# Performance work log

Hardware: AMD Instinct MI355X
Metric: run time of the kernel (lower is better)

Reference implementation:

```python
import jax, jax.numpy as jnp
import numpy as np

NL = 6        # num_layers
V = 512       # pad_vocab_size (d_model)
H = 8         # nhead
HD = V // H   # head dim
DFF = 2048    # dim_feedforward
MAXLEN = 1024 # max distance for relative-position embedding
B = 8
L = 1024
EPS = 1e-5


def _ln(x, g, b):
    m = jnp.mean(x, axis=-1, keepdims=True)
    v = jnp.mean(jnp.square(x - m), axis=-1, keepdims=True)
    return (x - m) * jax.lax.rsqrt(v + EPS) * g + b


def setup_inputs() -> dict:
    key = jax.random.key(0)
    ks = jax.random.split(key, 16)
    s = 0.02
    rn = lambda k, shp: (jax.random.normal(k, shp) * s).astype(jnp.float32)
    return {
        "x": jax.random.uniform(ks[0], (B, L, V), jnp.float32),
        "dist_emb": rn(ks[1], (MAXLEN + 1, H)),
        "in_proj_w": rn(ks[2], (NL, 3 * V, V)),
        "in_proj_b": rn(ks[3], (NL, 3 * V)),
        "out_w": rn(ks[4], (NL, V, V)),
        "out_b": rn(ks[5], (NL, V)),
        "lin1_w": rn(ks[6], (NL, DFF, V)),
        "lin1_b": rn(ks[7], (NL, DFF)),
        "lin2_w": rn(ks[8], (NL, V, DFF)),
        "lin2_b": rn(ks[9], (NL, V)),
        "ln1_g": jnp.ones((NL, V), jnp.float32),
        "ln1_b": jnp.zeros((NL, V), jnp.float32),
        "ln2_g": jnp.ones((NL, V), jnp.float32),
        "ln2_b": jnp.zeros((NL, V), jnp.float32),
        "lnf_g": jnp.ones((V,), jnp.float32),
        "lnf_b": jnp.zeros((V,), jnp.float32),
    }


def _forward(x, dist_emb, in_proj_w, in_proj_b, out_w, out_b,
             lin1_w, lin1_b, lin2_w, lin2_b,
             ln1_g, ln1_b, ln2_g, ln2_b, lnf_g, lnf_b):
    bsz, seqlen, _ = x.shape
    idx = jnp.arange(seqlen)
    dist = jnp.clip(jnp.abs(idx[None, :] - idx[:, None]), 0, MAXLEN)  # (L, L)
    bias = jnp.transpose(dist_emb[dist], (2, 0, 1))[None]  # (1, H, L, L)
    causal = idx[None, :] <= idx[:, None]                   # allow j <= i
    bias = jnp.where(causal[None, None], bias, -jnp.inf)
    kpm = ~jnp.any(x != 0, axis=2)                          # (B, L) key padding
    bias = jnp.where(kpm[:, None, None, :], -jnp.inf, bias)  # (B, H, L, L)

    out = x  # eval mode: dropouts are identity
    scale = 1.0 / np.sqrt(HD)
    for l in range(NL):
        # --- self attention (post-norm TransformerEncoderLayer) ---
        qkv = out @ in_proj_w[l].T + in_proj_b[l]            # (B, L, 3V)
        q, k, v = jnp.split(qkv, 3, axis=-1)
        q = q.reshape(bsz, seqlen, H, HD)
        k = k.reshape(bsz, seqlen, H, HD)
        v = v.reshape(bsz, seqlen, H, HD)
        scores = jnp.einsum('bqhd,bkhd->bhqk', q, k) * scale + bias
        probs = jax.nn.softmax(scores, axis=-1)
        attn = jnp.einsum('bhqk,bkhd->bqhd', probs, v).reshape(bsz, seqlen, V)
        attn = attn @ out_w[l].T + out_b[l]
        out = _ln(out + attn, ln1_g[l], ln1_b[l])
        # --- feed forward (gelu) ---
        h = jax.nn.gelu(out @ lin1_w[l].T + lin1_b[l], approximate=False)
        ff = h @ lin2_w[l].T + lin2_b[l]
        out = _ln(out + ff, ln2_g[l], ln2_b[l])
    return _ln(out, lnf_g, lnf_b)


def reference(x, dist_emb, in_proj_w, in_proj_b, out_w, out_b,
              lin1_w, lin1_b, lin2_w, lin2_b,
              ln1_g, ln1_b, ln2_g, ln2_b, lnf_g, lnf_b):
    return _forward(x, dist_emb, in_proj_w, in_proj_b, out_w, out_b,
                    lin1_w, lin1_b, lin2_w, lin2_b,
                    ln1_g, ln1_b, ln2_g, ln2_b, lnf_g, lnf_b)
```

## Files before the change

kernel.cpp:

```cpp
#include <hip/hip_runtime.h>
#include <hip/hip_bf16.h>
#include <math.h>

#define NL 6
#define V 512
#define H 8
#define HD 64
#define DFF 2048
#define MAXLEN 1024
#define B 8
#define L 1024
#define M (B*L)
#define EPS 1e-5f
#define LOG2E 1.44269504088896f

typedef __hip_bfloat16 bf16;
typedef __attribute__((ext_vector_type(8))) short s8v;
typedef __attribute__((ext_vector_type(4))) float f4v;

__device__ __forceinline__ float b2f(bf16 v){ return __bfloat162float(v); }
__device__ __forceinline__ bf16 f2b(float v){ return __float2bfloat16(v); }
__device__ __forceinline__ unsigned short f2bu(float v){
  return __builtin_bit_cast(unsigned short, __float2bfloat16(v));
}
__device__ __forceinline__ float usf(unsigned short u){
  union{unsigned int i; float f;} c; c.i = ((unsigned int)u)<<16; return c.f;
}

__device__ __forceinline__ float ldin(const void* p, size_t i, int bf){
  if(bf) return b2f(((const bf16*)p)[i]);
  return ((const float*)p)[i];
}

__device__ __forceinline__ void ldin8f(const void* p, size_t e, int bf, float* o){
  if(bf){
    union{uint4 v; unsigned short u[8];} c;
    c.v = *(const uint4*)((const bf16*)p + e);
    #pragma unroll
    for(int i=0;i<8;i++) o[i]=usf(c.u[i]);
  }else{
    const float* f=(const float*)p+e;
    float4 a=*(const float4*)f, b=*(const float4*)(f+4);
    o[0]=a.x;o[1]=a.y;o[2]=a.z;o[3]=a.w;o[4]=b.x;o[5]=b.y;o[6]=b.z;o[7]=b.w;
  }
}

__device__ __forceinline__ uint4 ldw8(const void* W, size_t e, int bf){
  if(bf) return *(const uint4*)((const bf16*)W + e);
  const float* p = (const float*)W + e;
  float4 f0 = *(const float4*)p;
  float4 f1 = *(const float4*)(p+4);
  union { unsigned short u[8]; uint4 v; } r;
  r.u[0]=f2bu(f0.x); r.u[1]=f2bu(f0.y); r.u[2]=f2bu(f0.z); r.u[3]=f2bu(f0.w);
  r.u[4]=f2bu(f1.x); r.u[5]=f2bu(f1.y); r.u[6]=f2bu(f1.z); r.u[7]=f2bu(f1.w);
  return r.v;
}

__device__ __forceinline__ void async16(const bf16* g, unsigned short* l){
  __builtin_amdgcn_global_load_lds((const __attribute__((address_space(1))) void*)g,
                                   (__attribute__((address_space(3))) void*)l, 16, 0, 0);
}

__global__ void k_detect(const void* ones, int* flag){
  unsigned int u = *(const unsigned int*)ones;
  flag[0] = (u == 0x3F803F80u) ? 1 : 0;
  flag[1] = 1;
}

__global__ __launch_bounds__(256) void k_conv(const void* __restrict__ src,
                                              bf16* __restrict__ dst,
                                              const int* __restrict__ flag, int n){
  int bf = *flag;
  int e = (blockIdx.x*256 + threadIdx.x)*8;
  if(e >= n) return;
  if(bf){
    *(uint4*)(dst+e) = *(const uint4*)((const bf16*)src + e);
  }else{
    const float* s = (const float*)src + e;
    float4 a = *(const float4*)s, b2 = *(const float4*)(s+4);
    union{uint4 v; unsigned short u[8];} c;
    c.u[0]=f2bu(a.x); c.u[1]=f2bu(a.y); c.u[2]=f2bu(a.z); c.u[3]=f2bu(a.w);
    c.u[4]=f2bu(b2.x);c.u[5]=f2bu(b2.y);c.u[6]=f2bu(b2.z);c.u[7]=f2bu(b2.w);
    *(uint4*)(dst+e) = c.v;
  }
}

__global__ __launch_bounds__(256) void k_cast_kpm(const void* __restrict__ x,
                                                 const int* __restrict__ flag,
                                                 bf16* __restrict__ cur,
                                                 float* __restrict__ kpm){
  int bf = *flag;
  int row = blockIdx.x; int t = threadIdx.x;
  __shared__ int nz;
  if(t==0) nz = 0;
  __syncthreads();
  int fl = 0;
  for(int e=t; e<V; e+=256){
    float f = ldin(x, (size_t)row*V+e, bf);
    cur[(size_t)row*V+e] = f2b(f);
    if(f != 0.f) fl = 1;
  }
  if(fl) atomicOr(&nz, 1);
  __syncthreads();
  if(t==0) kpm[row] = nz ? 0.f : 1.f;
}

template<int BN, int WM, int WN, int TM, int TN>
__global__ __launch_bounds__(256) void k_gemm(const bf16* __restrict__ A,
                                              const void* __restrict__ W,
                                              const void* __restrict__ bias,
                                              const int* __restrict__ flag,
                                              bf16* __restrict__ C,
                                              int Ndim, int K, int gelu,
                                              size_t w_off, size_t b_off){
  constexpr int TILE = (128+BN)*64;
  constexpr int ES  = BN + 8;
  __shared__ unsigned short lds[2*TILE];
  int bf = *flag;
  int t = threadIdx.x;
  int rb = blockIdx.x*128, cb = blockIdx.y*BN;
  int lane = t & 63, w = t >> 6;
  int wm = w % WM, wn = w / WM;
  int quad = lane >> 4, fid = lane & 15;

  f4v acc[TM][TN];
  #pragma unroll
  for(int i=0;i<TM;i++)
    #pragma unroll
    for(int j=0;j<TN;j++){ f4v z = {0.f,0.f,0.f,0.f}; acc[i][j] = z; }

  auto stage = [&](int kt, int bsel){
    unsigned short* Ad = lds + bsel*TILE;
    unsigned short* Bd = Ad + 128*64;
    int k0 = kt*64;
    #pragma unroll
    for(int i=0;i<4;i++){
      int r = w*32 + i*8 + (lane>>3);
      const bf16* g = A + (size_t)(rb+r)*K + k0 + (((lane&7)^(r&7))<<3);
      async16(g, Ad + (w*32 + i*8)*64);
    }
    if(bf){
      #pragma unroll
      for(int i=0;i<BN/32;i++){
        int r = w*(BN/4) + i*8 + (lane>>3);
        const bf16* g = (const bf16*)W + w_off + (size_t)(cb+r)*K + k0 + (((lane&7)^(r&7))<<3);
        async16(g, Bd + (w*(BN/4) + i*8)*64);
      }
    }else{
      const int tpr = 256/BN;
      int sr = t/tpr;
      int sc0 = (t%tpr)*(64/tpr);
      #pragma unroll
      for(int c=0;c<64/tpr;c+=8){
        uint4 d = ldw8(W, w_off + (size_t)(cb+sr)*K + k0 + sc0 + c, 0);
        int chunk = (sc0+c)>>3;
        *(uint4*)&Bd[sr*64 + ((chunk^(sr&7))<<3)] = d;
      }
    }
  };

  int KT = K/64;
  stage(0, 0);
  __syncthreads();
  int cur = 0;
  for(int kt=0;kt<KT;kt++){
    if(kt+1<KT) stage(kt+1, cur^1);
    unsigned short* As = lds + cur*TILE;
    unsigned short* Bs = As + 128*64;
    #pragma unroll
    for(int h=0;h<2;h++){
      s8v av[TM], bv[TN];
      #pragma unroll
      for(int tm=0;tm<TM;tm++){
        int r = wm*(TM*16) + tm*16 + fid;
        av[tm] = *(const s8v*)&As[r*64 + (((h*4+quad)^(r&7))<<3)];
      }
      #pragma unroll
      for(int tn=0;tn<TN;tn++){
        int c = wn*(TN*16) + tn*16 + fid;
        bv[tn] = *(const s8v*)&Bs[c*64 + (((h*4+quad)^(c&7))<<3)];
      }
      #pragma unroll
      for(int tm=0;tm<TM;tm++)
        #pragma unroll
        for(int tn=0;tn<TN;tn++)
          acc[tm][tn] = __builtin_amdgcn_mfma_f32_16x16x32_bf16(av[tm], bv[tn], acc[tm][tn], 0,0,0);
    }
    __syncthreads();
    cur ^= 1;
  }

  float bvv[TN];
  #pragma unroll
  for(int tn=0;tn<TN;tn++)
    bvv[tn] = ldin(bias, b_off + cb + wn*(TN*16) + tn*16 + fid, bf);
  unsigned short* E = lds;
  #pragma unroll
  for(int tn=0;tn<TN;tn++){
    int col = wn*(TN*16) + tn*16 + fid;
    #pragma unroll
    for(int tm=0;tm<TM;tm++)
      #pragma unroll
      for(int rg=0; rg<4; rg++){
        int row = wm*(TM*16) + tm*16 + quad*4 + rg;
        float v = acc[tm][tn][rg] + bvv[tn];
        if(gelu) v = 0.5f*v*(1.f+erff(v*0.70710678118f));
        E[row*ES + col] = f2bu(v);
      }
  }
  __syncthreads();
  int row = t>>1, c0 = (t&1)*(BN/2);
  bf16* cp = C + (size_t)(rb+row)*Ndim + cb + c0;
  #pragma unroll
  for(int c=0;c<BN/2;c+=8)
    *(uint4*)(cp + c) = *(const uint4*)&E[row*ES + c0 + c];
}

__global__ __launch_bounds__(256) void k_attn(const bf16* __restrict__ qkv,
                                              const void* __restrict__ dist_emb,
                                              const int* __restrict__ flag,
                                              const float* __restrict__ kpm,
                                              bf16* __restrict__ out){
  int bf = *flag;
  int t = threadIdx.x;
  int p = blockIdx.x;
  int bh = blockIdx.y; int b = bh>>3, h = bh&7;
  int w = t>>6, lane = t&63, quad = lane>>4, fid = lane&15;

  __shared__ unsigned short Ks[2][64][70];
  __shared__ unsigned short Vt[2][64][70];
  __shared__ unsigned short Ps[4][16][70];
  __shared__ float distc[L];
  __shared__ float kflagS[2][64];

  int qt0 = p, qt1 = 15-p;
  int dmax = (qt1+1)*64;
  for(int i=t;i<dmax;i+=256) distc[i] = ldin(dist_emb,(size_t)i*H+h,bf) * LOG2E;

  int r  = t>>2, dc = (t&3)*16;
  int d0 = (t&15)*4, jj = (t>>4)*4;
  uint4 kr0, kr1; uint2 vb[4]; float kf;

  auto loadrg = [&](int j0){
    size_t kbase = (size_t)(b*L+j0+r)*(3*V) + h*HD + dc;
    kr0 = *(const uint4*)(qkv + kbase + V);
    kr1 = *(const uint4*)(qkv + kbase + V + 8);
    #pragma unroll
    for(int k2=0;k2<4;k2++)
      vb[k2] = *(const uint2*)(qkv + (size_t)(b*L+j0+jj+k2)*(3*V) + 2*V + h*HD + d0);
    kf = (t < 64) ? kpm[b*L + j0 + t] : 0.f;
  };

  auto store_tile = [&](int d){
    *(uint4*)&Ks[d][r][dc]   = kr0;
    *(uint4*)&Ks[d][r][dc+8] = kr1;
    const unsigned short* v0 = (const unsigned short*)&vb[0];
    const unsigned short* v1 = (const unsigned short*)&vb[1];
    const unsigned short* v2 = (const unsigned short*)&vb[2];
    const unsigned short* v3 = (const unsigned short*)&vb[3];
    #pragma unroll
    for(int i2=0;i2<4;i2++){
      unsigned short o[4] = {v0[i2], v1[i2], v2[i2], v3[i2]};
      *(uint2*)&Vt[d][d0+i2][jj] = *(uint2*)o;
    }
    if(t < 64) kflagS[d][t] = kf;
  };

  auto loadQ = [&](int rb, s8v& a0, s8v& a1){
    int qrow = rb + w*16 + fid;
    const bf16* qp = qkv + (size_t)(b*L+qrow)*(3*V) + h*HD;
    a0 = *(const s8v*)(qp + quad*8);
    a1 = *(const s8v*)(qp + 32 + quad*8);
  };

  float mrow[4], lrow[4];
  f4v Oc[4];
  #pragma unroll
  for(int q2=0;q2<4;q2++){ mrow[q2]=-1e30f; lrow[q2]=0.f;
                           f4v z={0.f,0.f,0.f,0.f}; Oc[q2]=z; }

  auto writeOut = [&](int rb){
    float inv[4];
    #pragma unroll
    for(int rg=0;rg<4;rg++) inv[rg] = (lrow[rg]>0.f) ? 1.f/lrow[rg] : 0.f;
    #pragma unroll
    for(int nt=0;nt<4;nt++)
      #pragma unroll
      for(int rg=0;rg<4;rg++){
        int row = rb + w*16 + quad*4 + rg;
        out[(size_t)(b*L+row)*V + h*HD + nt*16 + fid] = f2b(Oc[nt][rg]*inv[rg]);
      }
  };

  int rb0 = qt0*64;
  s8v aq0, aq1;
  loadQ(rb0, aq0, aq1);

  loadrg(0);
  store_tile(0);
  __syncthreads();

  const int NTT = 17;
  for(int it=0; it<NTT; it++){
    int bufi = it & 1;
    int ph = (it > qt0);
    int qt = ph ? qt1 : qt0;
    int jt = ph ? (it - qt0 - 1) : it;
    int j0 = jt*64;
    if(it < NTT-1) loadrg((it==qt0) ? 0 : j0+64);

    f4v Sc[4];
    #pragma unroll
    for(int nt=0;nt<4;nt++){ f4v z={0.f,0.f,0.f,0.f}; Sc[nt]=z; }
    __builtin_amdgcn_s_setprio(1);
    #pragma unroll
    for(int nt=0;nt<4;nt++){
      s8v bk0 = *(const s8v*)&Ks[bufi][nt*16+fid][quad*8];
      s8v bk1 = *(const s8v*)&Ks[bufi][nt*16+fid][32+quad*8];
      Sc[nt] = __builtin_amdgcn_mfma_f32_16x16x32_bf16(aq0, bk0, Sc[nt], 0,0,0);
      Sc[nt] = __builtin_amdgcn_mfma_f32_16x16x32_bf16(aq1, bk1, Sc[nt], 0,0,0);
    }
    __builtin_amdgcn_s_setprio(0);

    int diag = (jt == qt);
    float sv[4][4];
    #pragma unroll
    for(int nt=0;nt<4;nt++){
      int col_j = j0 + nt*16 + fid;
      int kmask = (kflagS[bufi][nt*16+fid] != 0.f);
      #pragma unroll
      for(int rg=0;rg<4;rg++){
        int row_q = rb0 + w*16 + quad*4 + rg;
        int masked = kmask | (diag & (col_j > row_q));
        float bias = masked ? 0.f : distc[row_q - col_j];
        sv[nt][rg] = masked ? -1e30f : fmaf(Sc[nt][rg], 0.125f*LOG2E, bias);
      }
    }

    float alpha[4]; float nm[4]; int grow = 0;
    #pragma unroll
    for(int rg=0;rg<4;rg++){
      float tmax = fmaxf(fmaxf(sv[0][rg],sv[1][rg]),fmaxf(sv[2][rg],sv[3][rg]));
      #pragma unroll
      for(int m2=1;m2<16;m2<<=1) tmax = fmaxf(tmax, __shfl_xor(tmax, m2));
      nm[rg] = fmaxf(mrow[rg], tmax);
      grow |= (nm[rg] > mrow[rg]);
    }
    int growany = __any(grow);
    #pragma unroll
    for(int rg=0;rg<4;rg++){
      float mn = nm[rg];
      float msub = (mn <= -1e29f) ? 0.f : mn;
      alpha[rg] = growany ? __builtin_amdgcn_exp2f(mrow[rg] - msub) : 1.f;
      mrow[rg] = mn;
      float ps = 0.f;
      #pragma unroll
      for(int nt=0;nt<4;nt++){
        float pv = __builtin_amdgcn_exp2f(sv[nt][rg]-msub);
        sv[nt][rg] = pv;
        ps += pv;
      }
      #pragma unroll
      for(int m2=1;m2<16;m2<<=1) ps += __shfl_xor(ps, m2);
      lrow[rg] = lrow[rg]*alpha[rg] + ps;
    }
    if(growany){
      #pragma unroll
      for(int nt=0;nt<4;nt++)
        #pragma unroll
        for(int rg=0;rg<4;rg++)
          Oc[nt][rg] *= alpha[rg];
    }

    #pragma unroll
    for(int nt=0;nt<4;nt++)
      #pragma unroll
      for(int rg=0;rg<4;rg++)
        Ps[w][quad*4+rg][nt*16+fid] = f2bu(sv[nt][rg]);
    s8v ap0 = *(const s8v*)&Ps[w][fid][quad*8];
    s8v ap1 = *(const s8v*)&Ps[w][fid][32+quad*8];
    __builtin_amdgcn_s_setprio(1);
    #pragma unroll
    for(int nt=0;nt<4;nt++){
      s8v bv0 = *(const s8v*)&Vt[bufi][nt*16+fid][quad*8];
      s8v bv1 = *(const s8v*)&Vt[bufi][nt*16+fid][32+quad*8];
      Oc[nt] = __builtin_amdgcn_mfma_f32_16x16x32_bf16(ap0, bv0, Oc[nt], 0,0,0);
      Oc[nt] = __builtin_amdgcn_mfma_f32_16x16x32_bf16(ap1, bv1, Oc[nt], 0,0,0);
    }
    __builtin_amdgcn_s_setprio(0);

    if(it < NTT-1) store_tile(bufi^1);
    __syncthreads();

    if(it == qt0){
      writeOut(rb0);
      rb0 = qt1*64;
      loadQ(rb0, aq0, aq1);
      #pragma unroll
      for(int q2=0;q2<4;q2++){ mrow[q2]=-1e30f; lrow[q2]=0.f;
                               f4v z={0.f,0.f,0.f,0.f}; Oc[q2]=z; }
    }
  }
  writeOut(rb0);
}

__global__ __launch_bounds__(256) void k_ln(const bf16* __restrict__ a,
                                            const bf16* __restrict__ r,
                                            const void* __restrict__ g,
                                            const void* __restrict__ be,
                                            const int* __restrict__ flag,
                                            void* __restrict__ outp,
                                            int use_r, int final_out,
                                            size_t gb_off){
  int bf = *flag;
  int t = threadIdx.x, w = t>>6, lane = t&63;
  int row = blockIdx.x*4 + w;
  size_t o = (size_t)row*V + lane*8;
  union{uint4 v; unsigned short u[8];} ua;
  ua.v = *(const uint4*)(a + o);
  float v[8];
  #pragma unroll
  for(int i=0;i<8;i++) v[i] = usf(ua.u[i]);
  if(use_r){
    union{uint4 v; unsigned short u[8];} ur;
    ur.v = *(const uint4*)(r + o);
    #pragma unroll
    for(int i=0;i<8;i++) v[i] += usf(ur.u[i]);
  }
  float s=0.f, q=0.f;
  #pragma unroll
  for(int i=0;i<8;i++){ s += v[i]; q += v[i]*v[i]; }
  #pragma unroll
  for(int m=1;m<64;m<<=1){ s += __shfl_xor(s, m); q += __shfl_xor(q, m); }
  float mean = s * (1.f/V);
  float var  = q * (1.f/V) - mean*mean;
  float rstd = 1.f / sqrtf(var + EPS);
  float gv[8], bv[8], ov[8];
  ldin8f(g,  gb_off + lane*8, bf, gv);
  ldin8f(be, gb_off + lane*8, bf, bv);
  #pragma unroll
  for(int i=0;i<8;i++) ov[i] = (v[i]-mean)*rstd*gv[i] + bv[i];
  if(final_out && !bf){
    float* op = (float*)outp + o;
    *(float4*)op     = make_float4(ov[0],ov[1],ov[2],ov[3]);
    *(float4*)(op+4) = make_float4(ov[4],ov[5],ov[6],ov[7]);
  }else{
    union{uint4 v; unsigned short u[8];} c;
    #pragma unroll
    for(int i=0;i<8;i++) c.u[i] = f2bu(ov[i]);
    *(uint4*)((bf16*)outp + o) = c.v;
  }
}

extern "C" void kernel_launch(void* const* d_in, const int* in_sizes, int n_in,
                              void* d_out, int out_size, void* d_ws, size_t ws_size,
                              hipStream_t stream){
  const void* x         = d_in[0];
  const void* dist_emb  = d_in[1];
  const void* in_proj_w = d_in[2];
  const void* in_proj_b = d_in[3];
  const void* out_w     = d_in[4];
  const void* out_b     = d_in[5];
  const void* lin1_w    = d_in[6];
  const void* lin1_b    = d_in[7];
  const void* lin2_w    = d_in[8];
  const void* lin2_b    = d_in[9];
  const void* ln1_g     = d_in[10];
  const void* ln1_bb    = d_in[11];
  const void* ln2_g     = d_in[12];
  const void* ln2_bb    = d_in[13];
  const void* lnf_g     = d_in[14];
  const void* lnf_bb    = d_in[15];

  int*   flag    = (int*)d_ws;
  int*   flagOne = flag + 1;
  float* kpm  = (float*)((char*)d_ws + 256);
  bf16*  cur  = (bf16*)(kpm + M);
  bf16*  big  = cur + (size_t)M*V;
  bf16*  attn = big + (size_t)M*(3*V);
  bf16*  proj = big + (size_t)M*DFF;
  char*  base_end = (char*)(proj + (size_t)M*V);

  const size_t S_ipw = (size_t)NL*3*V*V, S_ow = (size_t)NL*V*V;
  const size_t S_l1w = (size_t)NL*DFF*V, S_l2w = (size_t)NL*V*DFF;
  const size_t S_ipb = (size_t)NL*3*V, S_ob = (size_t)NL*V;
  const size_t S_l1b = (size_t)NL*DFF, S_l2b = (size_t)NL*V;
  const size_t SW = S_ipw + S_ow + S_l1w + S_l2w;
  const size_t SB = S_ipb + S_ob + S_l1b + S_l2b;
  size_t need = (size_t)(base_end - (char*)d_ws) + (SW + SB)*sizeof(bf16);
  int conv = (ws_size >= need);

  bf16* w_ip = (bf16*)base_end;
  bf16* w_o  = w_ip + S_ipw;
  bf16* w_l1 = w_o  + S_ow;
  bf16* w_l2 = w_l1 + S_l1w;
  bf16* b_ip = w_l2 + S_l2w;
  bf16* b_o  = b_ip + S_ipb;
  bf16* b_l1 = b_o  + S_ob;
  bf16* b_l2 = b_l1 + S_l1b;

  k_detect<<<1, 1, 0, stream>>>(lnf_g, flag);
  k_cast_kpm<<<M, 256, 0, stream>>>(x, flag, cur, kpm);

  const int* gflag = conv ? flagOne : flag;
  const void* g_ipw = conv ? (const void*)w_ip : in_proj_w;
  const void* g_ow  = conv ? (const void*)w_o  : out_w;
  const void* g_l1w = conv ? (const void*)w_l1 : lin1_w;
  const void* g_l2w = conv ? (const void*)w_l2 : lin2_w;
  const void* g_ipb = conv ? (const void*)b_ip : in_proj_b;
  const void* g_ob  = conv ? (const void*)b_o  : out_b;
  const void* g_l1b = conv ? (const void*)b_l1 : lin1_b;
  const void* g_l2b = conv ? (const void*)b_l2 : lin2_b;

  if(conv){
    auto cv = [&](const void* s, bf16* d, size_t n){
      k_conv<<<(unsigned)((n/8 + 255)/256), 256, 0, stream>>>(s, d, flag, (int)n);
    };
    cv(in_proj_w, w_ip, S_ipw);  cv(out_w, w_o, S_ow);
    cv(lin1_w, w_l1, S_l1w);     cv(lin2_w, w_l2, S_l2w);
    cv(in_proj_b, b_ip, S_ipb);  cv(out_b, b_o, S_ob);
    cv(lin1_b, b_l1, S_l1b);     cv(lin2_b, b_l2, S_l2b);
  }

  for(int l=0;l<NL;l++){
    k_gemm<128,2,2,4,4><<<dim3(M/128, (3*V)/128), 256, 0, stream>>>(
        cur, g_ipw, g_ipb, gflag, big, 3*V, V, 0,
        (size_t)l*3*V*V, (size_t)l*3*V);
    k_attn<<<dim3(8, B*H), 256, 0, stream>>>(big, dist_emb, flag, kpm, attn);
    k_gemm<64,4,1,2,4><<<dim3(M/128, V/64), 256, 0, stream>>>(
        attn, g_ow, g_ob, gflag, proj, V, V, 0,
        (size_t)l*V*V, (size_t)l*V);
    k_ln<<<M/4, 256, 0, stream>>>(cur, proj, ln1_g, ln1_bb, flag, cur, 1, 0, (size_t)l*V);
    k_gemm<128,2,2,4,4><<<dim3(M/128, DFF/128), 256, 0, stream>>>(
        cur, g_l1w, g_l1b, gflag, big, DFF, V, 1,
        (size_t)l*DFF*V, (size_t)l*DFF);
    k_gemm<64,4,1,2,4><<<dim3(M/128, V/64), 256, 0, stream>>>(
        big, g_l2w, g_l2b, gflag, proj, V, DFF, 0,
        (size_t)l*V*DFF, (size_t)l*V);
    k_ln<<<M/4, 256, 0, stream>>>(cur, proj, ln2_g, ln2_bb, flag, cur, 1, 0, (size_t)l*V);
  }
  k_ln<<<M/4, 256, 0, stream>>>(cur, cur, lnf_g, lnf_bb, flag, d_out, 0, 1, 0);
}
```

Baseline: 1.261 ms.

## Split attention KV tiles across two warpgroups with split-K softmax merge

The attention kernel now launches 512 threads per block. Two 256-thread warpgroups each process alternating key tiles for the same query tile, each keeping its own online-softmax state, and the two partial results are merged through shared memory at the end of each query tile. The goal is to halve the serial KV loop length per block and raise occupancy and latency hiding on a grid of only 512 blocks. In exchange it adds a merge step, an extra barrier per iteration, and loses the double-buffered prefetch overlap, since each warpgroup now owns one K/V buffer.

```diff
diff --git a/kernel.cpp b/kernel.cpp
--- a/kernel.cpp
+++ b/kernel.cpp
@@ -216,7 +216,7 @@
     *(uint4*)(cp + c) = *(const uint4*)&E[row*ES + c0 + c];
 }
 
-__global__ __launch_bounds__(256) void k_attn(const bf16* __restrict__ qkv,
+__global__ __launch_bounds__(512) void k_attn(const bf16* __restrict__ qkv,
                                               const void* __restrict__ dist_emb,
                                               const int* __restrict__ flag,
                                               const float* __restrict__ kpm,
@@ -225,21 +225,33 @@
   int t = threadIdx.x;
   int p = blockIdx.x;
   int bh = blockIdx.y; int b = bh>>3, h = bh&7;
-  int w = t>>6, lane = t&63, quad = lane>>4, fid = lane&15;
+  int wg = t>>8, tg = t&255;
+  int w = tg>>6, lane = tg&63, quad = lane>>4, fid = lane&15;
+  int ww = t>>6;
 
   __shared__ unsigned short Ks[2][64][70];
   __shared__ unsigned short Vt[2][64][70];
-  __shared__ unsigned short Ps[4][16][70];
+  __shared__ unsigned short PsRaw[8*16*70];
   __shared__ float distc[L];
   __shared__ float kflagS[2][64];
+  __shared__ float mlX[4][16][2];
 
   int qt0 = p, qt1 = 15-p;
-  int dmax = (qt1+1)*64;
-  for(int i=t;i<dmax;i+=256) distc[i] = ldin(dist_emb,(size_t)i*H+h,bf) * LOG2E;
-
-  int r  = t>>2, dc = (t&3)*16;
-  int d0 = (t&15)*4, jj = (t>>4)*4;
+  int c0 = qt0+1, c1 = qt1+1;
+  int I0 = (c0+1)>>1, IT = I0 + ((c1+1)>>1);
+
+  int dmax = c1*64;
+  for(int i=t;i<dmax;i+=512) distc[i] = ldin(dist_emb,(size_t)i*H+h,bf) * LOG2E;
+
+  int r  = tg>>2, dc = (tg&3)*16;
+  int d0 = (tg&15)*4, jj = (tg>>4)*4;
   uint4 kr0, kr1; uint2 vb[4]; float kf;
+
+  auto tileJ = [&](int i)->int{
+    if(i < 0 || i >= IT) return -1;
+    if(i < I0){ int jt = 2*i + wg; return (jt < c0) ? jt : -1; }
+    int jt = 2*(i-I0) + wg; return (jt < c1) ? jt : -1;
+  };
 
   auto loadrg = [&](int j0){
     size_t kbase = (size_t)(b*L+j0+r)*(3*V) + h*HD + dc;
@@ -248,12 +260,12 @@
     #pragma unroll
     for(int k2=0;k2<4;k2++)
       vb[k2] = *(const uint2*)(qkv + (size_t)(b*L+j0+jj+k2)*(3*V) + 2*V + h*HD + d0);
-    kf = (t < 64) ? kpm[b*L + j0 + t] : 0.f;
+    kf = (tg < 64) ? kpm[b*L + j0 + tg] : 0.f;
   };
 
-  auto store_tile = [&](int d){
-    *(uint4*)&Ks[d][r][dc]   = kr0;
-    *(uint4*)&Ks[d][r][dc+8] = kr1;
+  auto store_tile = [&](){
+    *(uint4*)&Ks[wg][r][dc]   = kr0;
+    *(uint4*)&Ks[wg][r][dc+8] = kr1;
     const unsigned short* v0 = (const unsigned short*)&vb[0];
     const unsigned short* v1 = (const unsigned short*)&vb[1];
     const unsigned short* v2 = (const unsigned short*)&vb[2];
@@ -261,16 +273,17 @@
     #pragma unroll
     for(int i2=0;i2<4;i2++){
       unsigned short o[4] = {v0[i2], v1[i2], v2[i2], v3[i2]};
-      *(uint2*)&Vt[d][d0+i2][jj] = *(uint2*)o;
-    }
-    if(t < 64) kflagS[d][t] = kf;
+      *(uint2*)&Vt[wg][d0+i2][jj] = *(uint2*)o;
+    }
+    if(tg < 64) kflagS[wg][tg] = kf;
   };
 
-  auto loadQ = [&](int rb, s8v& a0, s8v& a1){
-    int qrow = rb + w*16 + fid;
+  s8v aq0, aq1;
+  auto loadQ = [&](int rbase){
+    int qrow = rbase + w*16 + fid;
     const bf16* qp = qkv + (size_t)(b*L+qrow)*(3*V) + h*HD;
-    a0 = *(const s8v*)(qp + quad*8);
-    a1 = *(const s8v*)(qp + 32 + quad*8);
+    aq0 = *(const s8v*)(qp + quad*8);
+    aq1 = *(const s8v*)(qp + 32 + quad*8);
   };
 
   float mrow[4], lrow[4];
@@ -279,129 +292,153 @@
   for(int q2=0;q2<4;q2++){ mrow[q2]=-1e30f; lrow[q2]=0.f;
                            f4v z={0.f,0.f,0.f,0.f}; Oc[q2]=z; }
 
-  auto writeOut = [&](int rb){
-    float inv[4];
-    #pragma unroll
-    for(int rg=0;rg<4;rg++) inv[rg] = (lrow[rg]>0.f) ? 1.f/lrow[rg] : 0.f;
-    #pragma unroll
-    for(int nt=0;nt<4;nt++)
+  float* Om = (float*)PsRaw;
+  auto mergeOut = [&](int rbase){
+    if(wg==1){
+      #pragma unroll
+      for(int nt=0;nt<4;nt++)
+        #pragma unroll
+        for(int rg=0;rg<4;rg++)
+          Om[(w*16 + quad*4+rg)*68 + nt*16+fid] = Oc[nt][rg];
+      if(fid==0){
+        #pragma unroll
+        for(int rg=0;rg<4;rg++){
+          mlX[w][quad*4+rg][0] = mrow[rg];
+          mlX[w][quad*4+rg][1] = lrow[rg];
+        }
+      }
+    }
+    __syncthreads();
+    if(wg==0){
       #pragma unroll
       for(int rg=0;rg<4;rg++){
-        int row = rb + w*16 + quad*4 + rg;
-        out[(size_t)(b*L+row)*V + h*HD + nt*16 + fid] = f2b(Oc[nt][rg]*inv[rg]);
-      }
+        float mB = mlX[w][quad*4+rg][0], lB = mlX[w][quad*4+rg][1];
+        float mM = fmaxf(mrow[rg], mB);
+        float msub = (mM <= -1e29f) ? 0.f : mM;
+        float sA = __builtin_amdgcn_exp2f(mrow[rg] - msub);
+        float sB = __builtin_amdgcn_exp2f(mB - msub);
+        float lm = lrow[rg]*sA + lB*sB;
+        float inv = (lm > 0.f) ? 1.f/lm : 0.f;
+        int row = rbase + w*16 + quad*4 + rg;
+        #pragma unroll
+        for(int nt=0;nt<4;nt++){
+          float ov = Oc[nt][rg]*sA + Om[(w*16 + quad*4+rg)*68 + nt*16+fid]*sB;
+          out[(size_t)(b*L+row)*V + h*HD + nt*16 + fid] = f2b(ov*inv);
+        }
+      }
+    }
   };
 
-  int rb0 = qt0*64;
-  s8v aq0, aq1;
-  loadQ(rb0, aq0, aq1);
-
-  loadrg(0);
-  store_tile(0);
+  int rb = qt0*64;
+  loadQ(rb);
+
+  { int j = tileJ(0); if(j>=0){ loadrg(j*64); store_tile(); }
+    j = tileJ(1); if(j>=0) loadrg(j*64); }
   __syncthreads();
 
-  const int NTT = 17;
-  for(int it=0; it<NTT; it++){
-    int bufi = it & 1;
-    int ph = (it > qt0);
+  for(int it=0; it<IT; it++){
+    int ph = (it >= I0);
     int qt = ph ? qt1 : qt0;
-    int jt = ph ? (it - qt0 - 1) : it;
-    int j0 = jt*64;
-    if(it < NTT-1) loadrg((it==qt0) ? 0 : j0+64);
-
-    f4v Sc[4];
-    #pragma unroll
-    for(int nt=0;nt<4;nt++){ f4v z={0.f,0.f,0.f,0.f}; Sc[nt]=z; }
-    __builtin_amdgcn_s_setprio(1);
-    #pragma unroll
-    for(int nt=0;nt<4;nt++){
-      s8v bk0 = *(const s8v*)&Ks[bufi][nt*16+fid][quad*8];
-      s8v bk1 = *(const s8v*)&Ks[bufi][nt*16+fid][32+quad*8];
-      Sc[nt] = __builtin_amdgcn_mfma_f32_16x16x32_bf16(aq0, bk0, Sc[nt], 0,0,0);
-      Sc[nt] = __builtin_amdgcn_mfma_f32_16x16x32_bf16(aq1, bk1, Sc[nt], 0,0,0);
-    }
-    __builtin_amdgcn_s_setprio(0);
-
-    int diag = (jt == qt);
-    float sv[4][4];
-    #pragma unroll
-    for(int nt=0;nt<4;nt++){
-      int col_j = j0 + nt*16 + fid;
-      int kmask = (kflagS[bufi][nt*16+fid] != 0.f);
+    int jt = tileJ(it);
+    if(jt >= 0){
+      int j0 = jt*64;
+      f4v Sc[4];
+      #pragma unroll
+      for(int nt=0;nt<4;nt++){ f4v z={0.f,0.f,0.f,0.f}; Sc[nt]=z; }
+      __builtin_amdgcn_s_setprio(1);
+      #pragma unroll
+      for(int nt=0;nt<4;nt++){
+        s8v bk0 = *(const s8v*)&Ks[wg][nt*16+fid][quad*8];
+        s8v bk1 = *(const s8v*)&Ks[wg][nt*16+fid][32+quad*8];
+        Sc[nt] = __builtin_amdgcn_mfma_f32_16x16x32_bf16(aq0, bk0, Sc[nt], 0,0,0);
+        Sc[nt] = __builtin_amdgcn_mfma_f32_16x16x32_bf16(aq1, bk1, Sc[nt], 0,0,0);
+      }
+      __builtin_amdgcn_s_setprio(0);
+
+      int diag = (jt == qt);
+      float sv[4][4];
+      #pragma unroll
+      for(int nt=0;nt<4;nt++){
+        int col_j = j0 + nt*16 + fid;
+        int kmask = (kflagS[wg][nt*16+fid] != 0.f);
+        #pragma unroll
+        for(int rg=0;rg<4;rg++){
+          int row_q = rb + w*16 + quad*4 + rg;
+          int masked = kmask | (diag & (col_j > row_q));
+          float bias = masked ? 0.f : distc[row_q - col_j];
+          sv[nt][rg] = masked ? -1e30f : fmaf(Sc[nt][rg], 0.125f*LOG2E, bias);
+        }
+      }
+
+      float alpha[4]; float nm[4]; int grow = 0;
       #pragma unroll
       for(int rg=0;rg<4;rg++){
-        int row_q = rb0 + w*16 + quad*4 + rg;
-        int masked = kmask | (diag & (col_j > row_q));
-        float bias = masked ? 0.f : distc[row_q - col_j];
-        sv[nt][rg] = masked ? -1e30f : fmaf(Sc[nt][rg], 0.125f*LOG2E, bias);
-      }
-    }
-
-    float alpha[4]; float nm[4]; int grow = 0;
-    #pragma unroll
-    for(int rg=0;rg<4;rg++){
-      float tmax = fmaxf(fmaxf(sv[0][rg],sv[1][rg]),fmaxf(sv[2][rg],sv[3][rg]));
-      #pragma unroll
-      for(int m2=1;m2<16;m2<<=1) tmax = fmaxf(tmax, __shfl_xor(tmax, m2));
-      nm[rg] = fmaxf(mrow[rg], tmax);
-      grow |= (nm[rg] > mrow[rg]);
-    }
-    int growany = __any(grow);
-    #pragma unroll
-    for(int rg=0;rg<4;rg++){
-      float mn = nm[rg];
-      float msub = (mn <= -1e29f) ? 0.f : mn;
-      alpha[rg] = growany ? __builtin_amdgcn_exp2f(mrow[rg] - msub) : 1.f;
-      mrow[rg] = mn;
-      float ps = 0.f;
+        float tmax = fmaxf(fmaxf(sv[0][rg],sv[1][rg]),fmaxf(sv[2][rg],sv[3][rg]));
+        #pragma unroll
+        for(int m2=1;m2<16;m2<<=1) tmax = fmaxf(tmax, __shfl_xor(tmax, m2));
+        nm[rg] = fmaxf(mrow[rg], tmax);
+        grow |= (nm[rg] > mrow[rg]);
+      }
+      int growany = __any(grow);
+      #pragma unroll
+      for(int rg=0;rg<4;rg++){
+        float mn = nm[rg];
+        float msub = (mn <= -1e29f) ? 0.f : mn;
+        alpha[rg] = growany ? __builtin_amdgcn_exp2f(mrow[rg] - msub) : 1.f;
+        mrow[rg] = mn;
+        float ps = 0.f;
+        #pragma unroll
+        for(int nt=0;nt<4;nt++){
+          float pv = __builtin_amdgcn_exp2f(sv[nt][rg]-msub);
+          sv[nt][rg] = pv;
+          ps += pv;
+        }
+        #pragma unroll
+        for(int m2=1;m2<16;m2<<=1) ps += __shfl_xor(ps, m2);
+        lrow[rg] = lrow[rg]*alpha[rg] + ps;
+      }
+      if(growany){
+        #pragma unroll
+        for(int nt=0;nt<4;nt++)
+          #pragma unroll
+          for(int rg=0;rg<4;rg++)
+            Oc[nt][rg] *= alpha[rg];
+      }
+
+      unsigned short* Ps = PsRaw + ww*16*70;
+      #pragma unroll
+      for(int nt=0;nt<4;nt++)
+        #pragma unroll
+        for(int rg=0;rg<4;rg++)
+          Ps[(quad*4+rg)*70 + nt*16+fid] = f2bu(sv[nt][rg]);
+      s8v ap0 = *(const s8v*)&Ps[fid*70 + quad*8];
+      s8v ap1 = *(const s8v*)&Ps[fid*70 + 32 + quad*8];
+      __builtin_amdgcn_s_setprio(1);
       #pragma unroll
       for(int nt=0;nt<4;nt++){
-        float pv = __builtin_amdgcn_exp2f(sv[nt][rg]-msub);
-        sv[nt][rg] = pv;
-        ps += pv;
-      }
-      #pragma unroll
-      for(int m2=1;m2<16;m2<<=1) ps += __shfl_xor(ps, m2);
-      lrow[rg] = lrow[rg]*alpha[rg] + ps;
-    }
-    if(growany){
-      #pragma unroll
-      for(int nt=0;nt<4;nt++)
-        #pragma unroll
-        for(int rg=0;rg<4;rg++)
-          Oc[nt][rg] *= alpha[rg];
-    }
-
-    #pragma unroll
-    for(int nt=0;nt<4;nt++)
-      #pragma unroll
-      for(int rg=0;rg<4;rg++)
-        Ps[w][quad*4+rg][nt*16+fid] = f2bu(sv[nt][rg]);
-    s8v ap0 = *(const s8v*)&Ps[w][fid][quad*8];
-    s8v ap1 = *(const s8v*)&Ps[w][fid][32+quad*8];
-    __builtin_amdgcn_s_setprio(1);
-    #pragma unroll
-    for(int nt=0;nt<4;nt++){
-      s8v bv0 = *(const s8v*)&Vt[bufi][nt*16+fid][quad*8];
-      s8v bv1 = *(const s8v*)&Vt[bufi][nt*16+fid][32+quad*8];
-      Oc[nt] = __builtin_amdgcn_mfma_f32_16x16x32_bf16(ap0, bv0, Oc[nt], 0,0,0);
-      Oc[nt] = __builtin_amdgcn_mfma_f32_16x16x32_bf16(ap1, bv1, Oc[nt], 0,0,0);
-    }
-    __builtin_amdgcn_s_setprio(0);
-
-    if(it < NTT-1) store_tile(bufi^1);
+        s8v bv0 = *(const s8v*)&Vt[wg][nt*16+fid][quad*8];
+        s8v bv1 = *(const s8v*)&Vt[wg][nt*16+fid][32+quad*8];
+        Oc[nt] = __builtin_amdgcn_mfma_f32_16x16x32_bf16(ap0, bv0, Oc[nt], 0,0,0);
+        Oc[nt] = __builtin_amdgcn_mfma_f32_16x16x32_bf16(ap1, bv1, Oc[nt], 0,0,0);
+      }
+      __builtin_amdgcn_s_setprio(0);
+    }
     __syncthreads();
 
-    if(it == qt0){
-      writeOut(rb0);
-      rb0 = qt1*64;
-      loadQ(rb0, aq0, aq1);
+    if(it == I0-1){
+      mergeOut(rb);
+      rb = qt1*64;
+      loadQ(rb);
       #pragma unroll
       for(int q2=0;q2<4;q2++){ mrow[q2]=-1e30f; lrow[q2]=0.f;
                                f4v z={0.f,0.f,0.f,0.f}; Oc[q2]=z; }
     }
-  }
-  writeOut(rb0);
+
+    { int jn = tileJ(it+1); if(jn>=0) store_tile();
+      int j2 = tileJ(it+2); if(j2>=0) loadrg(j2*64); }
+    __syncthreads();
+  }
+  mergeOut(rb);
 }
 
 __global__ __launch_bounds__(256) void k_ln(const bf16* __restrict__ a,
@@ -526,7 +563,7 @@
     k_gemm<128,2,2,4,4><<<dim3(M/128, (3*V)/128), 256, 0, stream>>>(
         cur, g_ipw, g_ipb, gflag, big, 3*V, V, 0,
         (size_t)l*3*V*V, (size_t)l*3*V);
-    k_attn<<<dim3(8, B*H), 256, 0, stream>>>(big, dist_emb, flag, kpm, attn);
+    k_attn<<<dim3(8, B*H), 512, 0, stream>>>(big, dist_emb, flag, kpm, attn);
     k_gemm<64,4,1,2,4><<<dim3(M/128, V/64), 256, 0, stream>>>(
         attn, g_ow, g_ob, gflag, proj, V, V, 0,
         (size_t)l*V*V, (size_t)l*V);
```

After: 1.252 ms. About the same (-0.7%).
